# Kernel optimization log

Measured on AMD Instinct MI355X. Metric: run time of the kernel, lower is better.

## Reference

```python
import jax, jax.numpy as jnp
import numpy as np

B = 64  # batch_size (number of graphs)


def _leaky(v):
    return jax.nn.leaky_relu(v, 0.01)


def _gine(x, src, dst, edge_attr, ew, eb, w1, b1, w2, b2):
    # GINEConv (eps=0): out = nn(x + sum_{j->i} relu(x_j + lin(edge_attr)))
    n = x.shape[0]
    msg = jax.nn.relu(x[src] + edge_attr @ ew + eb)      # [E, C]
    agg = jax.ops.segment_sum(msg, dst, num_segments=n)  # [N, C]
    h = x + agg
    h = _leaky(h @ w1 + b1)
    h = _leaky(h @ w2 + b2)
    return h


def setup_inputs() -> dict:
    key = jax.random.key(0)
    ks = jax.random.split(key, 32)
    N, E, NF, EF, H, A = 65536, 1048576, 32, 16, 128, 10
    s = 0.05
    inp = {
        'x': jax.random.normal(ks[0], (N, NF), jnp.float32),
        'edge_index': jax.random.randint(ks[1], (2, E), 0, N, jnp.int64)
        if jax.config.jax_enable_x64 else jax.random.randint(ks[1], (2, E), 0, N, jnp.int32),
        'edge_attr': jax.random.normal(ks[2], (E, EF), jnp.float32),
        'e1_w': jax.random.normal(ks[3], (EF, NF)) * s, 'e1_b': jnp.zeros((NF,)),
        'c1_w1': jax.random.normal(ks[4], (NF, H)) * s, 'c1_b1': jnp.zeros((H,)),
        'c1_w2': jax.random.normal(ks[5], (H, H)) * s, 'c1_b2': jnp.zeros((H,)),
        'e2_w': jax.random.normal(ks[6], (EF, H)) * s, 'e2_b': jnp.zeros((H,)),
        'c2_w1': jax.random.normal(ks[7], (H, H)) * s, 'c2_b1': jnp.zeros((H,)),
        'c2_w2': jax.random.normal(ks[8], (H, H)) * s, 'c2_b2': jnp.zeros((H,)),
        'a_w1': jax.random.normal(ks[9], (H, H)) * s, 'a_b1': jnp.zeros((H,)),
        'a_w2': jax.random.normal(ks[10], (H, A)) * s, 'a_b2': jnp.zeros((A,)),
        'n_w1': jax.random.normal(ks[11], (H, H)) * s, 'n_b1': jnp.zeros((H,)),
        'n_w2': jax.random.normal(ks[12], (H, H)) * s, 'n_b2': jnp.zeros((H,)),
        'n_w3': jax.random.normal(ks[13], (H, 1)) * s, 'n_b3': jnp.zeros((1,)),
    }
    return inp


def reference(x, edge_index, edge_attr,
              e1_w, e1_b, c1_w1, c1_b1, c1_w2, c1_b2,
              e2_w, e2_b, c2_w1, c2_b1, c2_w2, c2_b2,
              a_w1, a_b1, a_w2, a_b2,
              n_w1, n_b1, n_w2, n_b2, n_w3, n_b3):
    src, dst = edge_index[0], edge_index[1]
    h = _gine(x, src, dst, edge_attr, e1_w, e1_b, c1_w1, c1_b1, c1_w2, c1_b2)
    h = jax.nn.relu(h)  # dropout is identity in eval mode
    h = _gine(h, src, dst, edge_attr, e2_w, e2_b, c2_w1, c2_b1, c2_w2, c2_b2)
    H = h.shape[-1]
    hb = h.reshape(B, -1, H)            # [B, Nper, H]
    pooled = hb.mean(axis=1)            # [B, H]
    a = _leaky(_leaky(pooled @ a_w1 + a_b1) @ a_w2 + a_b2)
    action_prob = jax.nn.softmax(a, axis=1)
    # reinterpret flat node order as [Nper, B, H], as in the torch reshape
    xr = h.reshape(-1, B, H)
    nh = _leaky(xr @ n_w1 + n_b1)
    nh = _leaky(nh @ n_w2 + n_b2)
    node_scores = jax.nn.sigmoid(nh @ n_w3 + n_b3)[..., 0].T  # [B, Nper]
    return action_prob, node_scores
```

## Files before the change

### kernel.cpp

```cpp
#include <hip/hip_runtime.h>
#include <math.h>

#define NNODES 65536
#define NEDGES 1048576
#define NF 32
#define EF 16
#define HD 128
#define NACT 10
#define NB 64
#define NPER 1024

typedef unsigned short u16;
typedef float  vf2  __attribute__((ext_vector_type(2)));
typedef float  vf4  __attribute__((ext_vector_type(4)));
typedef __bf16 vbf8 __attribute__((ext_vector_type(8)));
#define BC8(v) __builtin_bit_cast(vbf8, v)
#define WB() __builtin_amdgcn_wave_barrier()

__device__ __forceinline__ float leakyf(float v) { return v > 0.0f ? v : 0.01f * v; }
__device__ __forceinline__ vf2 fma2(vf2 a, vf2 b, vf2 c) { return __builtin_elementwise_fma(a, b, c); }
__device__ __forceinline__ vf2 max2(vf2 a, vf2 b) { return __builtin_elementwise_max(a, b); }
__device__ __forceinline__ vf2 splat2(float s) { vf2 r = {s, s}; return r; }

__device__ __forceinline__ u16 f2bf(float x) {
    unsigned u = __float_as_uint(x);
    return (u16)((u + 0x7FFFu + ((u >> 16) & 1u)) >> 16);
}
__device__ __forceinline__ float bf2f(u16 h) { return __uint_as_float(((unsigned)h) << 16); }

__device__ __forceinline__ void cvt4(const float4 s, uint2& hi, uint2& lo) {
    const u16 h0 = f2bf(s.x), h1 = f2bf(s.y), h2 = f2bf(s.z), h3 = f2bf(s.w);
    hi = make_uint2((unsigned)h0 | ((unsigned)h1 << 16), (unsigned)h2 | ((unsigned)h3 << 16));
    const u16 l0 = f2bf(s.x - bf2f(h0)), l1 = f2bf(s.y - bf2f(h1));
    const u16 l2 = f2bf(s.z - bf2f(h2)), l3 = f2bf(s.w - bf2f(h3));
    lo = make_uint2((unsigned)l0 | ((unsigned)l1 << 16), (unsigned)l2 | ((unsigned)l3 << 16));
}
__device__ __forceinline__ uint2 cvt4hi(const float4 s) {
    const u16 h0 = f2bf(s.x), h1 = f2bf(s.y), h2 = f2bf(s.z), h3 = f2bf(s.w);
    return make_uint2((unsigned)h0 | ((unsigned)h1 << 16), (unsigned)h2 | ((unsigned)h3 << 16));
}

template<int K>
__device__ __forceinline__ void bcast16_fma(const float av, const vf2* __restrict__ wr, vf2& m) {
    const float a = __uint_as_float((unsigned)__builtin_amdgcn_ds_swizzle(
        (int)__float_as_uint(av), (K << 5) | 0x10));
    m = fma2(splat2(a), wr[K], m);
    if constexpr (K + 1 < EF) bcast16_fma<K + 1>(av, wr, m);
}

__global__ __launch_bounds__(256) void hist_kernel(const int* __restrict__ ei, int* __restrict__ cnt)
{
    const int i = blockIdx.x * 256 + threadIdx.x;
    if (i < NEDGES) atomicAdd(&cnt[ei[NEDGES + i]], 1);
}

__global__ __launch_bounds__(1024) void scan_kernel(const int* __restrict__ cnt, int* __restrict__ rs)
{
    __shared__ int s[1024];
    const int t = threadIdx.x;
    int loc[64];
    int tot = 0;
    const int4* c4 = (const int4*)(cnt + t * 64);
    #pragma unroll
    for (int j = 0; j < 16; ++j) {
        const int4 v = c4[j];
        loc[4*j+0] = v.x; loc[4*j+1] = v.y; loc[4*j+2] = v.z; loc[4*j+3] = v.w;
        tot += v.x + v.y + v.z + v.w;
    }
    s[t] = tot;
    __syncthreads();
    for (int off = 1; off < 1024; off <<= 1) {
        const int v = (t >= off) ? s[t - off] : 0;
        __syncthreads();
        s[t] += v;
        __syncthreads();
    }
    int run = s[t] - tot;
    #pragma unroll
    for (int j = 0; j < 64; ++j) { rs[t * 64 + j] = run; run += loc[j]; }
    if (t == 0) rs[NNODES] = NEDGES;
}

__global__ __launch_bounds__(256) void scatter_kernel(
    const int* __restrict__ ei, const int* __restrict__ rs, int* __restrict__ fill,
    int* __restrict__ ssrc, int* __restrict__ seidx)
{
    const int i = blockIdx.x * 256 + threadIdx.x;
    if (i < NEDGES) {
        const int d = ei[NEDGES + i];
        const int pos = rs[d] + atomicAdd(&fill[d], 1);
        ssrc[pos]  = ei[i];
        seidx[pos] = i;
    }
}

__global__ __launch_bounds__(256) void permute_kernel(
    const int* __restrict__ seidx, const float* __restrict__ ea, float* __restrict__ sea)
{
    const int t = blockIdx.x * 256 + threadIdx.x;
    const int e = t >> 2, part = t & 3;
    const int idx = seidx[e];
    ((float4*)sea)[(size_t)e * 4 + part] = ((const float4*)ea)[(size_t)idx * 4 + part];
}

__global__ __launch_bounds__(256) void pack_all_kernel(
    const float* __restrict__ w0, const float* __restrict__ w1, const float* __restrict__ w2,
    const float* __restrict__ w3, const float* __restrict__ w4, const float* __restrict__ w5,
    u16* __restrict__ pw)
{
    const int bid = blockIdx.x;
    const float* W; int KB, seg, sbase;
    if (bid < 16) { W = w0; KB = 1; seg = 0; sbase = 0; }
    else {
        const int i = (bid - 16) >> 6;
        seg = i + 1; sbase = 16 + i * 64; KB = 4;
        W = (i == 0) ? w1 : (i == 1) ? w2 : (i == 2) ? w3 : (i == 3) ? w4 : w5;
    }
    const int t = (bid - sbase) * 256 + threadIdx.x;
    const int j = t & 7, lane = (t >> 3) & 63, rest = t >> 9;
    const int kb = rest % KB, fb = rest / KB;
    if (fb >= 8) return;
    const int k = kb * 32 + (lane >> 4) * 8 + j;
    const int f = fb * 16 + (lane & 15);
    const float val = W[k * HD + f];
    const u16 h = f2bf(val);
    u16* dst = pw + seg * 32768;
    dst[t] = h;
    dst[16384 + t] = f2bf(val - bf2f(h));
}

__global__ __launch_bounds__(256) void e1_agg_kernel(
    const float* __restrict__ x, const int* __restrict__ rs,
    const int* __restrict__ ssrc, const float* __restrict__ sea,
    const float* __restrict__ w, const float* __restrict__ b, float* __restrict__ agg)
{
    const int tid  = threadIdx.x;
    const int lane = tid & 63;
    const int p    = lane & 15;
    const int q    = lane >> 4;
    const int node0 = (blockIdx.x * 4 + (tid >> 6)) * 4;
    vf2 wr[EF];
    #pragma unroll
    for (int k = 0; k < EF; ++k) wr[k] = *(const vf2*)&w[k * NF + p * 2];
    const vf2 bias = *(const vf2*)&b[p * 2];
    int rsv[5];
    #pragma unroll
    for (int i = 0; i < 5; ++i) rsv[i] = __builtin_amdgcn_readfirstlane(rs[node0 + i]);
    int srcLn[4];
    #pragma unroll
    for (int n = 0; n < 4; ++n) {
        const int nw0 = min(rsv[n + 1] - rsv[n], 64);
        srcLn[n] = (lane < nw0) ? ssrc[rsv[n] + lane] : 0;
    }
    #pragma unroll
    for (int n = 0; n < 4; ++n) {
        const int beg = rsv[n], end = rsv[n + 1];
        vf2 acc = {0.0f, 0.0f};
        int srcL = srcLn[n];
        for (int wnd = beg; wnd < end; wnd += 64) {
            const int nw = min(end - wnd, 64);
            if (wnd != beg) srcL = (lane < nw) ? ssrc[wnd + lane] : 0;
            const float* sbase = sea + (size_t)wnd * EF;
            int blk = 0;
            for (; blk + 16 <= nw; blk += 16) {
                float av[4];
                #pragma unroll
                for (int u = 0; u < 4; ++u)
                    av[u] = sbase[blk * EF + u * 64 + lane];
                vf2 xv[4];
                #pragma unroll
                for (int u = 0; u < 4; ++u) {
                    const int sA = __shfl(srcL, blk + u * 4 + q, 64);
                    xv[u] = *(const vf2*)((const char*)x + (((unsigned)sA << 7) + (unsigned)p * 8));
                }
                #pragma unroll
                for (int u = 0; u < 4; ++u) {
                    vf2 m = bias;
                    bcast16_fma<0>(av[u], wr, m);
                    acc += max2(xv[u] + m, splat2(0.0f));
                }
            }
            const int nrem = nw - blk;
            if (nrem > 0) {
                #pragma unroll
                for (int u = 0; u < 4; ++u) {
                    if (u * 4 >= nrem) break;
                    const int myidx = u * 4 + q;
                    const bool valid = myidx < nrem;
                    const float av = valid ? sbase[blk * EF + u * 64 + lane] : 0.0f;
                    const int sA = __shfl(srcL, min(blk + myidx, nw - 1), 64);
                    const vf2 xv = *(const vf2*)((const char*)x + (((unsigned)sA << 7) + (unsigned)p * 8));
                    vf2 m = bias;
                    bcast16_fma<0>(av, wr, m);
                    if (valid) acc += max2(xv + m, splat2(0.0f));
                }
            }
        }
        acc[0] += __shfl_xor(acc[0], 16, 64); acc[1] += __shfl_xor(acc[1], 16, 64);
        acc[0] += __shfl_xor(acc[0], 32, 64); acc[1] += __shfl_xor(acc[1], 32, 64);
        if (lane < 16) *(vf2*)&agg[(size_t)(node0 + n) * NF + p * 2] = acc;
    }
}

__global__ __launch_bounds__(256) void e2_agg_kernel(
    const float* __restrict__ h, const int* __restrict__ rs,
    const int* __restrict__ ssrc, const float* __restrict__ sea,
    const float* __restrict__ w, const float* __restrict__ b, float* __restrict__ agg)
{
    const int tid  = threadIdx.x;
    const int lane = tid & 63;
    const unsigned foff = (unsigned)lane * 8;
    const int node = blockIdx.x * 4 + (tid >> 6);
    vf2 wr[EF];
    #pragma unroll
    for (int k = 0; k < EF; ++k) wr[k] = *(const vf2*)&w[k * HD + lane * 2];
    const vf2 bias = *(const vf2*)&b[lane * 2];
    const int beg = __builtin_amdgcn_readfirstlane(rs[node]);
    const int end = __builtin_amdgcn_readfirstlane(rs[node + 1]);
    vf2 acc = {0.0f, 0.0f};
    int e = beg;
    #define LDH(s) (*(const vf2*)((const char*)h + (((unsigned)(s) << 9) + foff)))
    if (e + 4 <= end) {
        int s0 = ssrc[e], s1 = ssrc[e + 1], s2 = ssrc[e + 2], s3 = ssrc[e + 3];
        vf2 h0 = LDH(s0), h1 = LDH(s1), h2 = LDH(s2), h3 = LDH(s3);
        for (; e + 8 <= end; e += 4) {
            const int t0 = ssrc[e + 4], t1 = ssrc[e + 5], t2 = ssrc[e + 6], t3 = ssrc[e + 7];
            const vf2 g0 = LDH(t0), g1 = LDH(t1), g2 = LDH(t2), g3 = LDH(t3);
            const float* a0 = &sea[(size_t)e * EF];
            vf2 m0 = bias, m1 = bias, m2 = bias, m3 = bias;
            #pragma unroll
            for (int k = 0; k < EF; ++k) {
                m0 = fma2(splat2(a0[k]),      wr[k], m0);
                m1 = fma2(splat2(a0[16 + k]), wr[k], m1);
            }
            acc += max2(h0 + m0, splat2(0.0f));
            acc += max2(h1 + m1, splat2(0.0f));
            #pragma unroll
            for (int k = 0; k < EF; ++k) {
                m2 = fma2(splat2(a0[32 + k]), wr[k], m2);
                m3 = fma2(splat2(a0[48 + k]), wr[k], m3);
            }
            acc += max2(h2 + m2, splat2(0.0f));
            acc += max2(h3 + m3, splat2(0.0f));
            s0 = t0; s1 = t1; s2 = t2; s3 = t3;
            h0 = g0; h1 = g1; h2 = g2; h3 = g3;
        }
        {
            const float* a0 = &sea[(size_t)e * EF];
            vf2 m0 = bias, m1 = bias, m2 = bias, m3 = bias;
            #pragma unroll
            for (int k = 0; k < EF; ++k) {
                m0 = fma2(splat2(a0[k]),      wr[k], m0);
                m1 = fma2(splat2(a0[16 + k]), wr[k], m1);
            }
            acc += max2(h0 + m0, splat2(0.0f));
            acc += max2(h1 + m1, splat2(0.0f));
            #pragma unroll
            for (int k = 0; k < EF; ++k) {
                m2 = fma2(splat2(a0[32 + k]), wr[k], m2);
                m3 = fma2(splat2(a0[48 + k]), wr[k], m3);
            }
            acc += max2(h2 + m2, splat2(0.0f));
            acc += max2(h3 + m3, splat2(0.0f));
            e += 4;
        }
    }
    for (; e < end; ++e) {
        const int sA = ssrc[e];
        const vf2 hA = LDH(sA);
        const float* aA = &sea[(size_t)e * EF];
        vf2 mA = bias;
        #pragma unroll
        for (int k = 0; k < EF; ++k) mA = fma2(splat2(aA[k]), wr[k], mA);
        acc += max2(hA + mA, splat2(0.0f));
    }
    #undef LDH
    *(vf2*)&agg[(size_t)node * HD + lane * 2] = acc;
}

#define ROW128 272
#define ROW32  80

__device__ __forceinline__ void mfma_layer128_in(
    const unsigned char* __restrict__ aH, const unsigned char* __restrict__ aL,
    const u16* __restrict__ wH, const u16* __restrict__ wL,
    const float* __restrict__ bias, int lane, vf4* __restrict__ acc)
{
    const int quad = lane >> 4, fm = lane & 15;
    int4 Bh[4], Bl[4];
    #pragma unroll
    for (int kb = 0; kb < 4; ++kb) {
        Bh[kb] = *(const int4*)(aH + fm * ROW128 + kb * 64 + quad * 16);
        Bl[kb] = *(const int4*)(aL + fm * ROW128 + kb * 64 + quad * 16);
    }
    #pragma unroll
    for (int fb = 0; fb < 8; ++fb) {
        const float4 bv = *(const float4*)&bias[fb * 16 + quad * 4];
        vf4 a = {bv.x, bv.y, bv.z, bv.w};
        #pragma unroll
        for (int kb = 0; kb < 4; ++kb) {
            const int4 wh = *(const int4*)(wH + ((fb * 4 + kb) * 64 + lane) * 8);
            const int4 wl = *(const int4*)(wL + ((fb * 4 + kb) * 64 + lane) * 8);
            a = __builtin_amdgcn_mfma_f32_16x16x32_bf16(BC8(wh), BC8(Bl[kb]), a, 0, 0, 0);
            a = __builtin_amdgcn_mfma_f32_16x16x32_bf16(BC8(wl), BC8(Bh[kb]), a, 0, 0, 0);
            a = __builtin_amdgcn_mfma_f32_16x16x32_bf16(BC8(wh), BC8(Bh[kb]), a, 0, 0, 0);
        }
        acc[fb] = a;
    }
}

__device__ __forceinline__ void mfma_layer128_act(
    const unsigned char* __restrict__ aH,
    const u16* __restrict__ wH, const u16* __restrict__ wL,
    const float* __restrict__ bias, int lane, vf4* __restrict__ acc)
{
    const int quad = lane >> 4, fm = lane & 15;
    int4 Bh[4];
    #pragma unroll
    for (int kb = 0; kb < 4; ++kb)
        Bh[kb] = *(const int4*)(aH + fm * ROW128 + kb * 64 + quad * 16);
    #pragma unroll
    for (int fb = 0; fb < 8; ++fb) {
        const float4 bv = *(const float4*)&bias[fb * 16 + quad * 4];
        vf4 a = {bv.x, bv.y, bv.z, bv.w};
        #pragma unroll
        for (int kb = 0; kb < 4; ++kb) {
            const int4 wh = *(const int4*)(wH + ((fb * 4 + kb) * 64 + lane) * 8);
            const int4 wl = *(const int4*)(wL + ((fb * 4 + kb) * 64 + lane) * 8);
            a = __builtin_amdgcn_mfma_f32_16x16x32_bf16(BC8(wl), BC8(Bh[kb]), a, 0, 0, 0);
            a = __builtin_amdgcn_mfma_f32_16x16x32_bf16(BC8(wh), BC8(Bh[kb]), a, 0, 0, 0);
        }
        acc[fb] = a;
    }
}

__device__ __forceinline__ void mfma_layer32_in(
    const unsigned char* __restrict__ aH, const unsigned char* __restrict__ aL,
    const u16* __restrict__ wH, const u16* __restrict__ wL,
    const float* __restrict__ bias, int lane, vf4* __restrict__ acc)
{
    const int quad = lane >> 4, fm = lane & 15;
    const int4 Bh = *(const int4*)(aH + fm * ROW32 + quad * 16);
    const int4 Bl = *(const int4*)(aL + fm * ROW32 + quad * 16);
    #pragma unroll
    for (int fb = 0; fb < 8; ++fb) {
        const float4 bv = *(const float4*)&bias[fb * 16 + quad * 4];
        vf4 a = {bv.x, bv.y, bv.z, bv.w};
        const int4 wh = *(const int4*)(wH + (fb * 64 + lane) * 8);
        const int4 wl = *(const int4*)(wL + (fb * 64 + lane) * 8);
        a = __builtin_amdgcn_mfma_f32_16x16x32_bf16(BC8(wh), BC8(Bl), a, 0, 0, 0);
        a = __builtin_amdgcn_mfma_f32_16x16x32_bf16(BC8(wl), BC8(Bh), a, 0, 0, 0);
        a = __builtin_amdgcn_mfma_f32_16x16x32_bf16(BC8(wh), BC8(Bh), a, 0, 0, 0);
        acc[fb] = a;
    }
}

__device__ __forceinline__ void store_act_hi(
    unsigned char* __restrict__ aH, int lane, vf4* __restrict__ acc)
{
    const int quad = lane >> 4, fm = lane & 15;
    #pragma unroll
    for (int fb = 0; fb < 8; ++fb) {
        const float4 s = {leakyf(acc[fb][0]), leakyf(acc[fb][1]), leakyf(acc[fb][2]), leakyf(acc[fb][3])};
        acc[fb][0] = s.x; acc[fb][1] = s.y; acc[fb][2] = s.z; acc[fb][3] = s.w;
        *(uint2*)(aH + fm * ROW128 + fb * 32 + quad * 8) = cvt4hi(s);
    }
}

__global__ __launch_bounds__(256) void n1_kernel(
    const float* __restrict__ x, const float* __restrict__ agg,
    const u16* __restrict__ w1h, const u16* __restrict__ w1l, const float* __restrict__ b1,
    const u16* __restrict__ w2h, const u16* __restrict__ w2l, const float* __restrict__ b2,
    float* __restrict__ hout)
{
    __shared__ __align__(16) unsigned char smem[4][2560 + 16 * ROW128];
    const int tid = threadIdx.x, lane = tid & 63, wid = tid >> 6;
    const int quad = lane >> 4, fm = lane & 15;
    const int tile = blockIdx.x * 4 + wid;
    unsigned char* inH = smem[wid];
    unsigned char* inL = inH + 16 * ROW32;
    unsigned char* aH  = inH + 2560;
    const size_t base = (size_t)tile * 16 * NF;
    #pragma unroll
    for (int i = 0; i < 2; ++i) {
        const int flat = i * 64 + lane;
        const int node = flat >> 3, kq = flat & 7;
        const float4 xv = *(const float4*)&x[base + node * NF + kq * 4];
        const float4 av = *(const float4*)&agg[base + node * NF + kq * 4];
        const float4 s = {xv.x + av.x, xv.y + av.y, xv.z + av.z, xv.w + av.w};
        uint2 phi, plo;
        cvt4(s, phi, plo);
        *(uint2*)(inH + node * ROW32 + kq * 8) = phi;
        *(uint2*)(inL + node * ROW32 + kq * 8) = plo;
    }
    WB();
    vf4 acc[8];
    mfma_layer32_in(inH, inL, w1h, w1l, b1, lane, acc);
    WB();
    store_act_hi(aH, lane, acc);
    WB();
    mfma_layer128_act(aH, w2h, w2l, b2, lane, acc);
    const size_t ob = (size_t)tile * 16 * HD;
    #pragma unroll
    for (int fb = 0; fb < 8; ++fb) {
        const float4 o = {fmaxf(acc[fb][0], 0.0f), fmaxf(acc[fb][1], 0.0f),
                          fmaxf(acc[fb][2], 0.0f), fmaxf(acc[fb][3], 0.0f)};
        *(float4*)&hout[ob + fm * HD + fb * 16 + quad * 4] = o;
    }
}

__global__ __launch_bounds__(256) void n2_kernel(
    const float* __restrict__ h, const float* __restrict__ agg,
    const u16* __restrict__ w1h, const u16* __restrict__ w1l, const float* __restrict__ b1,
    const u16* __restrict__ w2h, const u16* __restrict__ w2l, const float* __restrict__ b2,
    const u16* __restrict__ m1h, const u16* __restrict__ m1l, const float* __restrict__ nb1,
    const u16* __restrict__ m2h, const u16* __restrict__ m2l, const float* __restrict__ nb2,
    const float* __restrict__ nw3, const float* __restrict__ nb3,
    float* __restrict__ pooled, float* __restrict__ scores)
{
    __shared__ __align__(16) unsigned char smem[4][2 * 16 * ROW128];
    const int tid = threadIdx.x, lane = tid & 63, wid = tid >> 6;
    const int quad = lane >> 4, fm = lane & 15;
    const int tile = blockIdx.x * 4 + wid;
    unsigned char* aH = smem[wid];
    unsigned char* aL = aH + 16 * ROW128;
    const size_t base = (size_t)tile * 16 * HD;
    #pragma unroll
    for (int i = 0; i < 8; ++i) {
        const int flat = i * 64 + lane;
        const int node = flat >> 5, kq = flat & 31;
        const float4 hv = *(const float4*)&h[base + node * HD + kq * 4];
        const float4 av = *(const float4*)&agg[base + node * HD + kq * 4];
        const float4 s = {hv.x + av.x, hv.y + av.y, hv.z + av.z, hv.w + av.w};
        uint2 phi, plo;
        cvt4(s, phi, plo);
        *(uint2*)(aH + node * ROW128 + kq * 8) = phi;
        *(uint2*)(aL + node * ROW128 + kq * 8) = plo;
    }
    WB();
    vf4 acc[8];
    mfma_layer128_in(aH, aL, w1h, w1l, b1, lane, acc);
    WB();
    store_act_hi(aH, lane, acc);
    WB();
    mfma_layer128_act(aH, w2h, w2l, b2, lane, acc);
    WB();
    store_act_hi(aH, lane, acc);
    {
        const int g = tile >> 6;
        #pragma unroll
        for (int fb = 0; fb < 8; ++fb) {
            vf4 t = acc[fb];
            #pragma unroll
            for (int off = 1; off < 16; off <<= 1) {
                t[0] += __shfl_xor(t[0], off, 64);
                t[1] += __shfl_xor(t[1], off, 64);
                t[2] += __shfl_xor(t[2], off, 64);
                t[3] += __shfl_xor(t[3], off, 64);
            }
            #pragma unroll
            for (int r = 0; r < 4; ++r) {
                const int item = fb * 4 + r;
                if (fm == (item >> 1))
                    atomicAdd(&pooled[g * HD + fb * 16 + quad * 4 + r], t[r]);
            }
        }
    }
    WB();
    mfma_layer128_act(aH, m1h, m1l, nb1, lane, acc);
    WB();
    store_act_hi(aH, lane, acc);
    WB();
    mfma_layer128_act(aH, m2h, m2l, nb2, lane, acc);
    float v = 0.0f;
    #pragma unroll
    for (int fb = 0; fb < 8; ++fb) {
        const float4 w3v = *(const float4*)&nw3[fb * 16 + quad * 4];
        v += leakyf(acc[fb][0]) * w3v.x + leakyf(acc[fb][1]) * w3v.y
           + leakyf(acc[fb][2]) * w3v.z + leakyf(acc[fb][3]) * w3v.w;
    }
    v += __shfl_xor(v, 16, 64);
    v += __shfl_xor(v, 32, 64);
    if (lane < 16) {
        const int node = tile * 16 + fm;
        const float s = v + nb3[0];
        scores[(node & 63) * NPER + (node >> 6)] = 1.0f / (1.0f + expf(-s));
    }
}

__global__ __launch_bounds__(128) void act_kernel(
    const float* __restrict__ pooled,
    const float* __restrict__ w1, const float* __restrict__ b1,
    const float* __restrict__ w2, const float* __restrict__ b2,
    float* __restrict__ out)
{
    __shared__ __align__(16) float p[HD];
    __shared__ float a1[HD];
    __shared__ float z[NACT];
    __shared__ float red2[2];
    const int g = blockIdx.x;
    const int tid = threadIdx.x;
    p[tid] = pooled[g * HD + tid] * (1.0f / NPER);
    __syncthreads();
    float acc = b1[tid];
    for (int k = 0; k < HD; ++k) acc = fmaf(p[k], w1[k * HD + tid], acc);
    a1[tid] = leakyf(acc);
    __syncthreads();
    if (tid < NACT) {
        float a2 = b2[tid];
        for (int k = 0; k < HD; ++k) a2 = fmaf(a1[k], w2[k * NACT + tid], a2);
        z[tid] = leakyf(a2);
    }
    __syncthreads();
    if (tid == 0) {
        float m = z[0];
        for (int i = 1; i < NACT; ++i) m = fmaxf(m, z[i]);
        red2[0] = m;
    }
    __syncthreads();
    if (tid < NACT) z[tid] = expf(z[tid] - red2[0]);
    __syncthreads();
    if (tid == 0) {
        float s = 0.0f;
        for (int i = 0; i < NACT; ++i) s += z[i];
        red2[1] = s;
    }
    __syncthreads();
    if (tid < NACT) out[g * NACT + tid] = z[tid] / red2[1];
}

extern "C" void kernel_launch(void* const* d_in, const int* in_sizes, int n_in,
                              void* d_out, int out_size, void* d_ws, size_t ws_size,
                              hipStream_t stream)
{
    const float* x    = (const float*)d_in[0];
    const int*   ei   = (const int*)d_in[1];
    const float* ea   = (const float*)d_in[2];
    const float* e1w  = (const float*)d_in[3];
    const float* e1b  = (const float*)d_in[4];
    const float* c1w1 = (const float*)d_in[5];
    const float* c1b1 = (const float*)d_in[6];
    const float* c1w2 = (const float*)d_in[7];
    const float* c1b2 = (const float*)d_in[8];
    const float* e2w  = (const float*)d_in[9];
    const float* e2b  = (const float*)d_in[10];
    const float* c2w1 = (const float*)d_in[11];
    const float* c2b1 = (const float*)d_in[12];
    const float* c2w2 = (const float*)d_in[13];
    const float* c2b2 = (const float*)d_in[14];
    const float* aw1  = (const float*)d_in[15];
    const float* ab1  = (const float*)d_in[16];
    const float* aw2  = (const float*)d_in[17];
    const float* ab2  = (const float*)d_in[18];
    const float* nw1  = (const float*)d_in[19];
    const float* nb1  = (const float*)d_in[20];
    const float* nw2  = (const float*)d_in[21];
    const float* nb2  = (const float*)d_in[22];
    const float* nw3  = (const float*)d_in[23];
    const float* nb3  = (const float*)d_in[24];

    float* out = (float*)d_out;
    char*  ws  = (char*)d_ws;
    const size_t MB = 1024 * 1024;
    float* h      = (float*)(ws);
    float* agg2   = (float*)(ws + 32  * MB);
    int*   seidx  = (int*)  (ws + 32  * MB);
    float* sea    = (float*)(ws + 64  * MB);
    float* agg1   = (float*)(ws + 128 * MB);
    float* pooled = (float*)(ws + 136 * MB);
    u16*   pw     = (u16*)  (ws + 136 * MB + 64 * 1024);
    int*   cnt    = (int*)  (ws + 137 * MB);
    int*   fill   = (int*)  (ws + 137 * MB + 256 * 1024);
    int*   rs     = (int*)  (ws + 139 * MB);
    int*   ssrc   = (int*)  (ws + 140 * MB);

    u16* p_c1w1 = pw;
    u16* p_c1w2 = pw + 1 * 32768;
    u16* p_c2w1 = pw + 2 * 32768;
    u16* p_c2w2 = pw + 3 * 32768;
    u16* p_nw1  = pw + 4 * 32768;
    u16* p_nw2  = pw + 5 * 32768;

    hipMemsetAsync(cnt,    0, 2 * NNODES * sizeof(int), stream);
    hipMemsetAsync(pooled, 0, (size_t)NB * HD * sizeof(float), stream);

    pack_all_kernel<<<336, 256, 0, stream>>>(c1w1, c1w2, c2w1, c2w2, nw1, nw2, pw);

    hist_kernel<<<NEDGES / 256, 256, 0, stream>>>(ei, cnt);
    scan_kernel<<<1, 1024, 0, stream>>>(cnt, rs);
    scatter_kernel<<<NEDGES / 256, 256, 0, stream>>>(ei, rs, fill, ssrc, seidx);
    permute_kernel<<<NEDGES / 64, 256, 0, stream>>>(seidx, ea, sea);

    e1_agg_kernel<<<NNODES / 16, 256, 0, stream>>>(x, rs, ssrc, sea, e1w, e1b, agg1);
    n1_kernel<<<NNODES / 64, 256, 0, stream>>>(x, agg1,
                                               p_c1w1, p_c1w1 + 16384, c1b1,
                                               p_c1w2, p_c1w2 + 16384, c1b2, h);
    e2_agg_kernel<<<NNODES / 4, 256, 0, stream>>>(h, rs, ssrc, sea, e2w, e2b, agg2);
    n2_kernel<<<NNODES / 64, 256, 0, stream>>>(h, agg2,
                                               p_c2w1, p_c2w1 + 16384, c2b1,
                                               p_c2w2, p_c2w2 + 16384, c2b2,
                                               p_nw1,  p_nw1  + 16384, nb1,
                                               p_nw2,  p_nw2  + 16384, nb2,
                                               nw3, nb3, pooled, out + NB * NACT);
    act_kernel<<<NB, 128, 0, stream>>>(pooled, aw1, ab1, aw2, ab2, out);
}
```

Measured before the change: 558.2 us.

## Gather bf16 node features in layer-2 aggregation and fuse edge permute into scatter

The first-layer node kernel now also writes a bf16 copy of h, and the second-layer edge aggregation gathers that copy. Each random gather then moves half the bytes, which targets the bandwidth of the dominant gather over 1M edges. Separately, the permute kernel is removed: scatter copies edge_attr rows straight to their CSR position, so the seidx round trip and one launch go away. The cost is bf16 rounding of x_j in the second-layer messages, plus scattered 64-byte writes in scatter.

```diff
diff --git a/kernel.cpp b/kernel.cpp
--- a/kernel.cpp
+++ b/kernel.cpp
@@ -28,6 +28,11 @@
 }
 __device__ __forceinline__ float bf2f(u16 h) { return __uint_as_float(((unsigned)h) << 16); }
 
+__device__ __forceinline__ vf2 up2(unsigned d) {
+    vf2 r = { __uint_as_float(d << 16), __uint_as_float(d & 0xFFFF0000u) };
+    return r;
+}
+
 __device__ __forceinline__ void cvt4(const float4 s, uint2& hi, uint2& lo) {
     const u16 h0 = f2bf(s.x), h1 = f2bf(s.y), h2 = f2bf(s.z), h3 = f2bf(s.w);
     hi = make_uint2((unsigned)h0 | ((unsigned)h1 << 16), (unsigned)h2 | ((unsigned)h3 << 16));
@@ -83,24 +88,18 @@
 
 __global__ __launch_bounds__(256) void scatter_kernel(
     const int* __restrict__ ei, const int* __restrict__ rs, int* __restrict__ fill,
-    int* __restrict__ ssrc, int* __restrict__ seidx)
+    int* __restrict__ ssrc, const float* __restrict__ ea, float* __restrict__ sea)
 {
     const int i = blockIdx.x * 256 + threadIdx.x;
     if (i < NEDGES) {
         const int d = ei[NEDGES + i];
         const int pos = rs[d] + atomicAdd(&fill[d], 1);
-        ssrc[pos]  = ei[i];
-        seidx[pos] = i;
-    }
-}
-
-__global__ __launch_bounds__(256) void permute_kernel(
-    const int* __restrict__ seidx, const float* __restrict__ ea, float* __restrict__ sea)
-{
-    const int t = blockIdx.x * 256 + threadIdx.x;
-    const int e = t >> 2, part = t & 3;
-    const int idx = seidx[e];
-    ((float4*)sea)[(size_t)e * 4 + part] = ((const float4*)ea)[(size_t)idx * 4 + part];
+        ssrc[pos] = ei[i];
+        const float4* src = (const float4*)ea + (size_t)i * 4;
+        const float4 a0 = src[0], a1 = src[1], a2 = src[2], a3 = src[3];
+        float4* dst = (float4*)sea + (size_t)pos * 4;
+        dst[0] = a0; dst[1] = a1; dst[2] = a2; dst[3] = a3;
+    }
 }
 
 __global__ __launch_bounds__(256) void pack_all_kernel(
@@ -203,13 +202,13 @@
 }
 
 __global__ __launch_bounds__(256) void e2_agg_kernel(
-    const float* __restrict__ h, const int* __restrict__ rs,
+    const u16* __restrict__ h16, const int* __restrict__ rs,
     const int* __restrict__ ssrc, const float* __restrict__ sea,
     const float* __restrict__ w, const float* __restrict__ b, float* __restrict__ agg)
 {
     const int tid  = threadIdx.x;
     const int lane = tid & 63;
-    const unsigned foff = (unsigned)lane * 8;
+    const unsigned foff = (unsigned)lane * 4;
     const int node = blockIdx.x * 4 + (tid >> 6);
     vf2 wr[EF];
     #pragma unroll
@@ -219,13 +218,13 @@
     const int end = __builtin_amdgcn_readfirstlane(rs[node + 1]);
     vf2 acc = {0.0f, 0.0f};
     int e = beg;
-    #define LDH(s) (*(const vf2*)((const char*)h + (((unsigned)(s) << 9) + foff)))
+    #define LDH(s) (*(const unsigned*)((const char*)h16 + (((unsigned)(s) << 8) + foff)))
     if (e + 4 <= end) {
         int s0 = ssrc[e], s1 = ssrc[e + 1], s2 = ssrc[e + 2], s3 = ssrc[e + 3];
-        vf2 h0 = LDH(s0), h1 = LDH(s1), h2 = LDH(s2), h3 = LDH(s3);
+        unsigned d0 = LDH(s0), d1 = LDH(s1), d2 = LDH(s2), d3 = LDH(s3);
         for (; e + 8 <= end; e += 4) {
             const int t0 = ssrc[e + 4], t1 = ssrc[e + 5], t2 = ssrc[e + 6], t3 = ssrc[e + 7];
-            const vf2 g0 = LDH(t0), g1 = LDH(t1), g2 = LDH(t2), g3 = LDH(t3);
+            const unsigned g0 = LDH(t0), g1 = LDH(t1), g2 = LDH(t2), g3 = LDH(t3);
             const float* a0 = &sea[(size_t)e * EF];
             vf2 m0 = bias, m1 = bias, m2 = bias, m3 = bias;
             #pragma unroll
@@ -233,17 +232,17 @@
                 m0 = fma2(splat2(a0[k]),      wr[k], m0);
                 m1 = fma2(splat2(a0[16 + k]), wr[k], m1);
             }
-            acc += max2(h0 + m0, splat2(0.0f));
-            acc += max2(h1 + m1, splat2(0.0f));
+            acc += max2(up2(d0) + m0, splat2(0.0f));
+            acc += max2(up2(d1) + m1, splat2(0.0f));
             #pragma unroll
             for (int k = 0; k < EF; ++k) {
                 m2 = fma2(splat2(a0[32 + k]), wr[k], m2);
                 m3 = fma2(splat2(a0[48 + k]), wr[k], m3);
             }
-            acc += max2(h2 + m2, splat2(0.0f));
-            acc += max2(h3 + m3, splat2(0.0f));
+            acc += max2(up2(d2) + m2, splat2(0.0f));
+            acc += max2(up2(d3) + m3, splat2(0.0f));
             s0 = t0; s1 = t1; s2 = t2; s3 = t3;
-            h0 = g0; h1 = g1; h2 = g2; h3 = g3;
+            d0 = g0; d1 = g1; d2 = g2; d3 = g3;
         }
         {
             const float* a0 = &sea[(size_t)e * EF];
@@ -253,26 +252,26 @@
                 m0 = fma2(splat2(a0[k]),      wr[k], m0);
                 m1 = fma2(splat2(a0[16 + k]), wr[k], m1);
             }
-            acc += max2(h0 + m0, splat2(0.0f));
-            acc += max2(h1 + m1, splat2(0.0f));
+            acc += max2(up2(d0) + m0, splat2(0.0f));
+            acc += max2(up2(d1) + m1, splat2(0.0f));
             #pragma unroll
             for (int k = 0; k < EF; ++k) {
                 m2 = fma2(splat2(a0[32 + k]), wr[k], m2);
                 m3 = fma2(splat2(a0[48 + k]), wr[k], m3);
             }
-            acc += max2(h2 + m2, splat2(0.0f));
-            acc += max2(h3 + m3, splat2(0.0f));
+            acc += max2(up2(d2) + m2, splat2(0.0f));
+            acc += max2(up2(d3) + m3, splat2(0.0f));
             e += 4;
         }
     }
     for (; e < end; ++e) {
         const int sA = ssrc[e];
-        const vf2 hA = LDH(sA);
+        const unsigned dA = LDH(sA);
         const float* aA = &sea[(size_t)e * EF];
         vf2 mA = bias;
         #pragma unroll
         for (int k = 0; k < EF; ++k) mA = fma2(splat2(aA[k]), wr[k], mA);
-        acc += max2(hA + mA, splat2(0.0f));
+        acc += max2(up2(dA) + mA, splat2(0.0f));
     }
     #undef LDH
     *(vf2*)&agg[(size_t)node * HD + lane * 2] = acc;
@@ -371,7 +370,7 @@
     const float* __restrict__ x, const float* __restrict__ agg,
     const u16* __restrict__ w1h, const u16* __restrict__ w1l, const float* __restrict__ b1,
     const u16* __restrict__ w2h, const u16* __restrict__ w2l, const float* __restrict__ b2,
-    float* __restrict__ hout)
+    float* __restrict__ hout, u16* __restrict__ hb16)
 {
     __shared__ __align__(16) unsigned char smem[4][2560 + 16 * ROW128];
     const int tid = threadIdx.x, lane = tid & 63, wid = tid >> 6;
@@ -406,6 +405,8 @@
         const float4 o = {fmaxf(acc[fb][0], 0.0f), fmaxf(acc[fb][1], 0.0f),
                           fmaxf(acc[fb][2], 0.0f), fmaxf(acc[fb][3], 0.0f)};
         *(float4*)&hout[ob + fm * HD + fb * 16 + quad * 4] = o;
+        *(uint2*)((unsigned char*)hb16 + (((size_t)(tile * 16 + fm)) << 8) + fb * 32 + quad * 8)
+            = cvt4hi(o);
     }
 }
 
@@ -564,7 +565,6 @@
     const size_t MB = 1024 * 1024;
     float* h      = (float*)(ws);
     float* agg2   = (float*)(ws + 32  * MB);
-    int*   seidx  = (int*)  (ws + 32  * MB);
     float* sea    = (float*)(ws + 64  * MB);
     float* agg1   = (float*)(ws + 128 * MB);
     float* pooled = (float*)(ws + 136 * MB);
@@ -573,6 +573,7 @@
     int*   fill   = (int*)  (ws + 137 * MB + 256 * 1024);
     int*   rs     = (int*)  (ws + 139 * MB);
     int*   ssrc   = (int*)  (ws + 140 * MB);
+    u16*   hb16   = (u16*)  (ws + 144 * MB);
 
     u16* p_c1w1 = pw;
     u16* p_c1w2 = pw + 1 * 32768;
@@ -588,14 +589,13 @@
 
     hist_kernel<<<NEDGES / 256, 256, 0, stream>>>(ei, cnt);
     scan_kernel<<<1, 1024, 0, stream>>>(cnt, rs);
-    scatter_kernel<<<NEDGES / 256, 256, 0, stream>>>(ei, rs, fill, ssrc, seidx);
-    permute_kernel<<<NEDGES / 64, 256, 0, stream>>>(seidx, ea, sea);
+    scatter_kernel<<<NEDGES / 256, 256, 0, stream>>>(ei, rs, fill, ssrc, ea, sea);
 
     e1_agg_kernel<<<NNODES / 16, 256, 0, stream>>>(x, rs, ssrc, sea, e1w, e1b, agg1);
     n1_kernel<<<NNODES / 64, 256, 0, stream>>>(x, agg1,
                                                p_c1w1, p_c1w1 + 16384, c1b1,
-                                               p_c1w2, p_c1w2 + 16384, c1b2, h);
-    e2_agg_kernel<<<NNODES / 4, 256, 0, stream>>>(h, rs, ssrc, sea, e2w, e2b, agg2);
+                                               p_c1w2, p_c1w2 + 16384, c1b2, h, hb16);
+    e2_agg_kernel<<<NNODES / 4, 256, 0, stream>>>(hb16, rs, ssrc, sea, e2w, e2b, agg2);
     n2_kernel<<<NNODES / 64, 256, 0, stream>>>(h, agg2,
                                                p_c2w1, p_c2w1 + 16384, c2b1,
                                                p_c2w2, p_c2w2 + 16384, c2b2,
```

Result: no change. 552.8 us (-1.0%).
